# Optimization experiments

Measured on AMD Instinct MI355X. Metric: run time of the kernel, lower is better.

Reference implementation:

```python
import jax, jax.numpy as jnp
import numpy as np

N_EMBD = 1024
BLOCK_SIZE = 2048
ATTN_SPAN = 256
LN_EPS = 1e-5


def _band_mask(T, span, dtype):
    ones = jnp.ones((T, T), dtype=dtype)
    # tril(.,0) * (1 - tril(.,-span)) -> causal band of width `span`
    return jnp.tril(ones, 0) * (1.0 - jnp.tril(ones, -span))


def setup_inputs() -> dict:
    key = jax.random.key(0)
    k_x, k_w, k_b, k_lw = jax.random.split(key, 4)
    B, T, C = 4, BLOCK_SIZE, N_EMBD
    x = jax.random.normal(k_x, (B, T, C), dtype=jnp.float32)
    # qkv_net: Linear(C, 3C) with bias (torch default)
    lim = 1.0 / np.sqrt(C)
    W_qkv = jax.random.uniform(k_w, (C, 3 * C), minval=-lim, maxval=lim, dtype=jnp.float32)
    b_qkv = jax.random.uniform(k_b, (3 * C,), minval=-lim, maxval=lim, dtype=jnp.float32)
    ln_w = jnp.ones((C,), dtype=jnp.float32)
    ln_b = jnp.zeros((C,), dtype=jnp.float32)
    return {"x": x, "W_qkv": W_qkv, "b_qkv": b_qkv, "ln_w": ln_w, "ln_b": ln_b}


def _layer_norm(h, w, b):
    mu = jnp.mean(h, axis=-1, keepdims=True)
    var = jnp.var(h, axis=-1, keepdims=True)
    return (h - mu) * jax.lax.rsqrt(var + LN_EPS) * w + b


def reference(x, W_qkv, b_qkv, ln_w, ln_b):
    B, T, C = x.shape
    qkv = x @ W_qkv + b_qkv  # [B,T,3C]
    q, k, v = jnp.split(qkv, 3, axis=-1)
    scale = np.sqrt(C * ATTN_SPAN).astype(np.float32)
    scores = jnp.einsum('bid,bjd->bij', q, k) / scale  # [B,T,T]
    scores = scores * _band_mask(T, ATTN_SPAN, x.dtype)[None, :, :]
    out = jnp.einsum('bij,bjd->bid', scores, v)  # [B,T,C]
    return _layer_norm(out, ln_w, ln_b)
```

## Files before the change

kernel.cpp:

```cpp
#include <hip/hip_runtime.h>
#include <cstdint>
#include <cstddef>

#define N_EMBD 1024
#define T_SEQ  2048
#define NBATCH 4
#define SPAN   256
#define C3     3072

typedef float  floatx4 __attribute__((ext_vector_type(4)));
typedef __bf16 bf16x8  __attribute__((ext_vector_type(8)));

__device__ inline unsigned short f2bf(float f) {
    union { float f; unsigned u; } x; x.f = f;
    unsigned u = x.u;
    unsigned r = (u + 0x7fffu + ((u >> 16) & 1u)) >> 16;
    return (unsigned short)r;
}

typedef __attribute__((address_space(1))) const void GVOID;
typedef __attribute__((address_space(3))) void LVOID;
__device__ inline void gl2lds16(const void* g, void* l) {
    __builtin_amdgcn_global_load_lds((GVOID*)g, (LVOID*)l, 16, 0, 0);
}

__device__ inline void stage128x32(const unsigned short* g, size_t stride,
                                   unsigned short* lds, int lane, int wave) {
    const int r     = wave * 16 + (lane >> 2);
    const int chunk = (lane & 3) ^ ((r >> 1) & 3);
    const unsigned short* src = g + (size_t)r * stride + chunk * 8;
    gl2lds16(src,               &lds[(wave * 16) * 32]);
    gl2lds16(src + 64 * stride, &lds[(64 + wave * 16) * 32]);
}

__device__ inline void stage64x64(const unsigned short* g, size_t stride,
                                  unsigned short* lds, int lane, int wave) {
#pragma unroll
    for (int rnd = 0; rnd < 2; rnd++) {
        const int r = rnd * 32 + wave * 8 + (lane >> 3);
        const int chunk = (lane & 7) ^ (r & 7);
        gl2lds16(g + (size_t)r * stride + chunk * 8, &lds[(rnd * 32 + wave * 8) * 64]);
    }
}

__device__ inline void stage128x64(const unsigned short* g, size_t stride,
                                   unsigned short* lds, int lane, int wave) {
#pragma unroll
    for (int rnd = 0; rnd < 4; rnd++) {
        const int r = rnd * 32 + wave * 8 + (lane >> 3);
        const int chunk = (lane & 7) ^ (r & 7);
        gl2lds16(g + (size_t)r * stride + chunk * 8, &lds[(rnd * 32 + wave * 8) * 64]);
    }
}

__global__ __launch_bounds__(256) void k_prep(const float* __restrict__ x,
                                              unsigned short* __restrict__ Xb,
                                              const float* __restrict__ W,
                                              unsigned short* __restrict__ WbT) {
    __shared__ unsigned short t[32][33];
    if (blockIdx.x < 8192) {
        int i = (blockIdx.x * 256 + threadIdx.x) * 4;
        float4 v = *(const float4*)(x + i);
        ushort4 o;
        o.x = f2bf(v.x); o.y = f2bf(v.y); o.z = f2bf(v.z); o.w = f2bf(v.w);
        *(ushort4*)(Xb + i) = o;
    } else {
        int bid = blockIdx.x - 8192;
        int k0 = (bid & 31) * 32, n0 = (bid >> 5) * 32;
        int tx = threadIdx.x & 31, ty = threadIdx.x >> 5;
#pragma unroll
        for (int i = 0; i < 4; i++) {
            int k = k0 + ty + i * 8;
            t[ty + i * 8][tx] = f2bf(W[(size_t)k * C3 + n0 + tx]);
        }
        __syncthreads();
#pragma unroll
        for (int i = 0; i < 4; i++) {
            int n = n0 + ty + i * 8;
            WbT[(size_t)n * N_EMBD + k0 + tx] = t[tx][ty + i * 8];
        }
    }
}

__global__ __launch_bounds__(256) void k_gemm(const unsigned short* __restrict__ Xb,
                                              const unsigned short* __restrict__ WbT,
                                              const float* __restrict__ bqkv,
                                              unsigned short* __restrict__ QK,
                                              unsigned short* __restrict__ Vt) {
    __shared__ unsigned short As[4096];
    __shared__ unsigned short Bs[4096];
    const int tid = threadIdx.x, lane = tid & 63, wave = tid >> 6;
    const int bx = blockIdx.x, m0 = blockIdx.y * 128;
    const bool isV = (bx >= 16);
    const int n0 = isV ? (2048 + (bx - 16) * 128) : (bx * 128);
    const int wr = wave >> 1, wc = wave & 1;

    floatx4 acc[4][4] = {};

    const unsigned short* gA = (isV ? WbT + (size_t)n0 * N_EMBD : Xb  + (size_t)m0 * N_EMBD);
    const unsigned short* gB = (isV ? Xb  + (size_t)m0 * N_EMBD : WbT + (size_t)n0 * N_EMBD);
    const int qk = ((lane >> 4) ^ ((lane >> 1) & 3)) * 8;
    const int ra = wr * 64 + (lane & 15);
    const int rb = wc * 64 + (lane & 15);

    for (int k0 = 0; k0 < N_EMBD; k0 += 32) {
        stage128x32(gA + k0, N_EMBD, As, lane, wave);
        stage128x32(gB + k0, N_EMBD, Bs, lane, wave);
        __syncthreads();
        bf16x8 a[4], b[4];
#pragma unroll
        for (int mi = 0; mi < 4; mi++) a[mi] = *(const bf16x8*)&As[(ra + mi * 16) * 32 + qk];
#pragma unroll
        for (int ni = 0; ni < 4; ni++) b[ni] = *(const bf16x8*)&Bs[(rb + ni * 16) * 32 + qk];
#pragma unroll
        for (int mi = 0; mi < 4; mi++)
#pragma unroll
            for (int ni = 0; ni < 4; ni++)
                acc[mi][ni] = __builtin_amdgcn_mfma_f32_16x16x32_bf16(a[mi], b[ni], acc[mi][ni], 0, 0, 0);
        __syncthreads();
    }

    const int cn = lane & 15, q = lane >> 4;
    unsigned short* base = isV ? Vt : QK;
    const int rowbase = isV ? (((m0 >> 11) << 10) + (n0 - 2048)) : m0;
    const int colbase = isV ? (m0 & 2047) : n0;
#pragma unroll
    for (int mi = 0; mi < 4; mi++) {
#pragma unroll
        for (int r = 0; r < 4; r++) {
            const int arow = wr * 64 + mi * 16 + q * 4 + r;
            unsigned short* dst = base + (size_t)(rowbase + arow) * 2048 + colbase;
#pragma unroll
            for (int ni = 0; ni < 4; ni++) {
                const int acol = wc * 64 + ni * 16 + cn;
                const float bias = bqkv[n0 + (isV ? arow : acol)];
                dst[acol] = f2bf(acc[mi][ni][r] + bias);
            }
        }
    }
}

__global__ __launch_bounds__(256) void k_scores(const unsigned short* __restrict__ QK,
                                                unsigned short* __restrict__ S) {
    const int jj = blockIdx.x, qb = blockIdx.y, b = blockIdx.z;
    const int jb = qb - 4 + jj;
    if (jb < 0) return;

    __shared__ unsigned short Qs[4096];
    __shared__ unsigned short Ks[4096];
    const int tid = threadIdx.x, lane = tid & 63, wave = tid >> 6;
    const int wr = wave >> 1, wc = wave & 1;
    const int n15 = lane & 15, q = lane >> 4;

    floatx4 acc[2][2] = {};

    const unsigned short* gQ = QK + ((size_t)(b * T_SEQ + qb * 64)) * 2048;
    const unsigned short* gK = QK + ((size_t)(b * T_SEQ + jb * 64)) * 2048 + 1024;

    for (int k0 = 0; k0 < N_EMBD; k0 += 64) {
        stage64x64(gQ + k0, 2048, Qs, lane, wave);
        stage64x64(gK + k0, 2048, Ks, lane, wave);
        __syncthreads();
#pragma unroll
        for (int s = 0; s < 2; s++) {
            bf16x8 a[2], bbf[2];
#pragma unroll
            for (int mi = 0; mi < 2; mi++) {
                const int row = wr * 32 + mi * 16 + n15;
                a[mi] = *(const bf16x8*)&Qs[row * 64 + (((s * 4 + q) ^ (row & 7)) * 8)];
            }
#pragma unroll
            for (int ni = 0; ni < 2; ni++) {
                const int row = wc * 32 + ni * 16 + n15;
                bbf[ni] = *(const bf16x8*)&Ks[row * 64 + (((s * 4 + q) ^ (row & 7)) * 8)];
            }
#pragma unroll
            for (int mi = 0; mi < 2; mi++)
#pragma unroll
                for (int ni = 0; ni < 2; ni++)
                    acc[mi][ni] = __builtin_amdgcn_mfma_f32_16x16x32_bf16(a[mi], bbf[ni], acc[mi][ni], 0, 0, 0);
        }
        __syncthreads();
    }

    unsigned short* Sb = S + (((size_t)(b * 32 + qb) * 5 + jj) << 12);
#pragma unroll
    for (int mi = 0; mi < 2; mi++)
#pragma unroll
        for (int ni = 0; ni < 2; ni++)
#pragma unroll
            for (int r = 0; r < 4; r++) {
                const int il = wr * 32 + mi * 16 + q * 4 + r;
                const int jl = wc * 32 + ni * 16 + n15;
                const int gi = qb * 64 + il, gj = jb * 64 + jl;
                const float v = ((gj <= gi) && (gj > gi - SPAN)) ? acc[mi][ni][r] * (1.0f / 512.0f) : 0.0f;
                Sb[il * 64 + jl] = f2bf(v);
            }
}

__global__ __launch_bounds__(256) void k_sv(const unsigned short* __restrict__ S,
                                            const unsigned short* __restrict__ Vt,
                                            float* __restrict__ out) {
    const int cg = blockIdx.x, qb = blockIdx.y, b = blockIdx.z;
    const int c0 = cg * 128;

    __shared__ unsigned short Ss[4096];
    __shared__ unsigned short Vs[8192];
    const int tid = threadIdx.x, lane = tid & 63, wave = tid >> 6;
    const int wr = wave >> 1, wc = wave & 1;
    const int n15 = lane & 15, q = lane >> 4;

    floatx4 acc[2][4] = {};

    for (int jj = 0; jj < 5; jj++) {
        const int jb = qb - 4 + jj;
        if (jb < 0) continue;
        stage64x64(S + (((size_t)(b * 32 + qb) * 5 + jj) << 12), 64, Ss, lane, wave);
        stage128x64(Vt + ((size_t)(b * 1024 + c0)) * 2048 + jb * 64, 2048, Vs, lane, wave);
        __syncthreads();
#pragma unroll
        for (int s = 0; s < 2; s++) {
            bf16x8 a[2], bbf[4];
#pragma unroll
            for (int mi = 0; mi < 2; mi++) {
                const int row = wr * 32 + mi * 16 + n15;
                a[mi] = *(const bf16x8*)&Ss[row * 64 + (((s * 4 + q) ^ (row & 7)) * 8)];
            }
#pragma unroll
            for (int ni = 0; ni < 4; ni++) {
                const int row = wc * 64 + ni * 16 + n15;
                bbf[ni] = *(const bf16x8*)&Vs[row * 64 + (((s * 4 + q) ^ (row & 7)) * 8)];
            }
#pragma unroll
            for (int mi = 0; mi < 2; mi++)
#pragma unroll
                for (int ni = 0; ni < 4; ni++)
                    acc[mi][ni] = __builtin_amdgcn_mfma_f32_16x16x32_bf16(a[mi], bbf[ni], acc[mi][ni], 0, 0, 0);
        }
        __syncthreads();
    }

#pragma unroll
    for (int mi = 0; mi < 2; mi++)
#pragma unroll
        for (int ni = 0; ni < 4; ni++)
#pragma unroll
            for (int r = 0; r < 4; r++) {
                const int il = wr * 32 + mi * 16 + q * 4 + r;
                const int cl = wc * 64 + ni * 16 + n15;
                out[((size_t)(b * T_SEQ + qb * 64 + il)) * N_EMBD + c0 + cl] = acc[mi][ni][r];
            }
}

__global__ __launch_bounds__(256) void k_ln(float* __restrict__ out,
                                            const float* __restrict__ w,
                                            const float* __restrict__ bias) {
    __shared__ float red[8];
    const int t = threadIdx.x;
    float* p = out + (size_t)blockIdx.x * N_EMBD;
    float4 v = ((const float4*)p)[t];
    float s  = v.x + v.y + v.z + v.w;
    float sq = v.x * v.x + v.y * v.y + v.z * v.z + v.w * v.w;
#pragma unroll
    for (int off = 32; off; off >>= 1) {
        s  += __shfl_down(s, off, 64);
        sq += __shfl_down(sq, off, 64);
    }
    const int wave = t >> 6, lane = t & 63;
    if (lane == 0) { red[wave] = s; red[4 + wave] = sq; }
    __syncthreads();
    const float ts = red[0] + red[1] + red[2] + red[3];
    const float tq = red[4] + red[5] + red[6] + red[7];
    const float mean = ts * (1.0f / N_EMBD);
    const float var  = tq * (1.0f / N_EMBD) - mean * mean;
    const float rs = rsqrtf(var + 1e-5f);
    float4 wv = ((const float4*)w)[t];
    float4 bv = ((const float4*)bias)[t];
    float4 o;
    o.x = (v.x - mean) * rs * wv.x + bv.x;
    o.y = (v.y - mean) * rs * wv.y + bv.y;
    o.z = (v.z - mean) * rs * wv.z + bv.z;
    o.w = (v.w - mean) * rs * wv.w + bv.w;
    ((float4*)p)[t] = o;
}

extern "C" void kernel_launch(void* const* d_in, const int* in_sizes, int n_in,
                              void* d_out, int out_size, void* d_ws, size_t ws_size,
                              hipStream_t stream) {
    const float* x  = (const float*)d_in[0];
    const float* W  = (const float*)d_in[1];
    const float* bq = (const float*)d_in[2];
    const float* lw = (const float*)d_in[3];
    const float* lb = (const float*)d_in[4];
    float* out = (float*)d_out;
    char* ws = (char*)d_ws;

    unsigned short* Xb   = (unsigned short*)(ws + 0);
    unsigned short* Sbuf = (unsigned short*)(ws + 0);
    unsigned short* WbT  = (unsigned short*)(ws + 16777216);
    unsigned short* QK   = (unsigned short*)(ws + 23068672);
    unsigned short* Vt   = (unsigned short*)(ws + 56623104);

    k_prep   <<<11264,           256, 0, stream>>>(x, Xb, W, WbT);
    k_gemm   <<<dim3(24, 64),    256, 0, stream>>>(Xb, WbT, bq, QK, Vt);
    k_scores <<<dim3(5, 32, 4),  256, 0, stream>>>(QK, Sbuf);
    k_sv     <<<dim3(8, 32, 4),  256, 0, stream>>>(Sbuf, Vt, out);
    k_ln     <<<8192,            256, 0, stream>>>(out, lw, lb);
}
```

Measured before the change: 207.5 us.

## Rewrite QKV GEMM with 256x128 tiles, double-buffered LDS and interleaved MFMA

The QKV projection GEMM moves from a single-buffered 128x128 tile with K=32 steps and 256 threads to a 256x128 tile with 512 threads. It uses K=64 steps and double-buffered LDS, issuing async global-to-LDS loads between MFMA groups with setprio and sched barriers. A workgroup index remap spreads tiles across XCDs. The aim is to hide global-load latency behind matrix math and raise arithmetic intensity. In exchange it brings a larger LDS footprint (96KB), more barriers, and hand-tuned vmcnt waits that must be exactly right.

Result: slower. 235.1 us (+13.3%).

```diff
diff --git a/kernel.cpp b/kernel.cpp
--- a/kernel.cpp
+++ b/kernel.cpp
@@ -24,13 +24,22 @@
     __builtin_amdgcn_global_load_lds((GVOID*)g, (LVOID*)l, 16, 0, 0);
 }
 
-__device__ inline void stage128x32(const unsigned short* g, size_t stride,
-                                   unsigned short* lds, int lane, int wave) {
-    const int r     = wave * 16 + (lane >> 2);
-    const int chunk = (lane & 3) ^ ((r >> 1) & 3);
-    const unsigned short* src = g + (size_t)r * stride + chunk * 8;
-    gl2lds16(src,               &lds[(wave * 16) * 32]);
-    gl2lds16(src + 64 * stride, &lds[(64 + wave * 16) * 32]);
+
+__device__ inline void stage_half128(const unsigned short* g, size_t stride,
+                                     unsigned short* lds, int lane, int wave) {
+#pragma unroll
+    for (int rnd = 0; rnd < 2; rnd++) {
+        const int r = rnd * 64 + wave * 8 + (lane >> 3);
+        const int chunk = (lane & 7) ^ (r & 7);
+        gl2lds16(g + (size_t)r * stride + chunk * 8, &lds[(rnd * 64 + wave * 8) * 64]);
+    }
+}
+
+__device__ inline void stage_half64(const unsigned short* g, size_t stride,
+                                    unsigned short* lds, int lane, int wave) {
+    const int r = wave * 8 + (lane >> 3);
+    const int chunk = (lane & 7) ^ (r & 7);
+    gl2lds16(g + (size_t)r * stride + chunk * 8, &lds[(wave * 8) * 64]);
 }
 
 __device__ inline void stage64x64(const unsigned short* g, size_t stride,
@@ -51,6 +60,10 @@
         const int chunk = (lane & 7) ^ (r & 7);
         gl2lds16(g + (size_t)r * stride + chunk * 8, &lds[(rnd * 32 + wave * 8) * 64]);
     }
+}
+
+__device__ inline bf16x8 frag_ld(const unsigned short* buf, int row, int ks, int q) {
+    return *(const bf16x8*)&buf[row * 64 + (((ks * 4 + q) ^ (row & 7)) * 8)];
 }
 
 __global__ __launch_bounds__(256) void k_prep(const float* __restrict__ x,
@@ -82,58 +95,154 @@
     }
 }
 
-__global__ __launch_bounds__(256) void k_gemm(const unsigned short* __restrict__ Xb,
+__global__ __launch_bounds__(512) void k_gemm(const unsigned short* __restrict__ Xb,
                                               const unsigned short* __restrict__ WbT,
                                               const float* __restrict__ bqkv,
                                               unsigned short* __restrict__ QK,
                                               unsigned short* __restrict__ Vt) {
-    __shared__ unsigned short As[4096];
-    __shared__ unsigned short Bs[4096];
+    __shared__ unsigned short As[2][256 * 64];
+    __shared__ unsigned short Bs[2][128 * 64];
     const int tid = threadIdx.x, lane = tid & 63, wave = tid >> 6;
-    const int bx = blockIdx.x, m0 = blockIdx.y * 128;
-    const bool isV = (bx >= 16);
-    const int n0 = isV ? (2048 + (bx - 16) * 128) : (bx * 128);
-    const int wr = wave >> 1, wc = wave & 1;
-
-    floatx4 acc[4][4] = {};
-
-    const unsigned short* gA = (isV ? WbT + (size_t)n0 * N_EMBD : Xb  + (size_t)m0 * N_EMBD);
-    const unsigned short* gB = (isV ? Xb  + (size_t)m0 * N_EMBD : WbT + (size_t)n0 * N_EMBD);
-    const int qk = ((lane >> 4) ^ ((lane >> 1) & 3)) * 8;
-    const int ra = wr * 64 + (lane & 15);
-    const int rb = wc * 64 + (lane & 15);
-
-    for (int k0 = 0; k0 < N_EMBD; k0 += 32) {
-        stage128x32(gA + k0, N_EMBD, As, lane, wave);
-        stage128x32(gB + k0, N_EMBD, Bs, lane, wave);
-        __syncthreads();
-        bf16x8 a[4], b[4];
-#pragma unroll
-        for (int mi = 0; mi < 4; mi++) a[mi] = *(const bf16x8*)&As[(ra + mi * 16) * 32 + qk];
-#pragma unroll
-        for (int ni = 0; ni < 4; ni++) b[ni] = *(const bf16x8*)&Bs[(rb + ni * 16) * 32 + qk];
-#pragma unroll
-        for (int mi = 0; mi < 4; mi++)
-#pragma unroll
-            for (int ni = 0; ni < 4; ni++)
-                acc[mi][ni] = __builtin_amdgcn_mfma_f32_16x16x32_bf16(a[mi], b[ni], acc[mi][ni], 0, 0, 0);
-        __syncthreads();
-    }
-
-    const int cn = lane & 15, q = lane >> 4;
+    const int wm = wave >> 2, wn = wave & 3;
+    const int n15 = lane & 15, q = lane >> 4;
+
+    const int wg = (blockIdx.x & 7) * 96 + (blockIdx.x >> 3);
+    const bool isV = (wg >= 512);
+
+    const unsigned short* gA;
+    const unsigned short* gB;
+    int rowbase, colbase, nb;
+    if (!isV) {
+        const int mt = wg >> 4, nt = wg & 15;
+        gA = Xb + (size_t)(mt * 256) * N_EMBD;
+        gB = WbT + (size_t)(nt * 128) * N_EMBD;
+        rowbase = mt * 256; colbase = nt * 128; nb = nt * 128;
+    } else {
+        const int v = wg - 512;
+        const int ct = v >> 6, tv = v & 63;
+        const int t0 = tv * 128;
+        gA = WbT + (size_t)(2048 + ct * 256) * N_EMBD;
+        gB = Xb + (size_t)t0 * N_EMBD;
+        rowbase = (t0 >> 11) * 1024 + ct * 256;
+        colbase = t0 & 2047;
+        nb = 2048 + ct * 256;
+    }
+
+    floatx4 acc[8][2] = {};
+
+#define BAR __builtin_amdgcn_s_barrier()
+#define MFMA8(MIBASE, NI)                                                          \
+    __builtin_amdgcn_sched_barrier(0);                                             \
+    __builtin_amdgcn_s_setprio(1);                                                 \
+    _Pragma("unroll")                                                              \
+    for (int ks = 0; ks < 2; ++ks)                                                 \
+        _Pragma("unroll")                                                          \
+        for (int mi = 0; mi < 4; ++mi)                                             \
+            acc[(MIBASE) + mi][NI] = __builtin_amdgcn_mfma_f32_16x16x32_bf16(      \
+                a[mi][ks], b[NI][ks], acc[(MIBASE) + mi][NI], 0, 0, 0);            \
+    __builtin_amdgcn_s_setprio(0);                                                 \
+    __builtin_amdgcn_sched_barrier(0);
+
+    stage_half128(gA,                    N_EMBD, As[0],            lane, wave);
+    stage_half128(gA + 128 * N_EMBD,     N_EMBD, As[0] + 128 * 64, lane, wave);
+    stage_half64 (gB,                    N_EMBD, Bs[0],            lane, wave);
+    stage_half64 (gB + 64 * N_EMBD,      N_EMBD, Bs[0] + 64 * 64,  lane, wave);
+    stage_half64 (gB + 64,               N_EMBD, Bs[1],            lane, wave);
+    stage_half64 (gB + 64 + 64 * N_EMBD, N_EMBD, Bs[1] + 64 * 64,  lane, wave);
+    asm volatile("s_waitcnt vmcnt(2)" ::: "memory");
+    BAR;
+
+#pragma unroll 1
+    for (int it = 0; it < 8; ++it) {
+        const int t0k = it * 128;
+        const int t1k = t0k + 64;
+        const bool last = (it == 7);
+        bf16x8 a[4][2], b[2][2];
+
+#pragma unroll
+        for (int mi = 0; mi < 4; ++mi)
+#pragma unroll
+            for (int ks = 0; ks < 2; ++ks)
+                a[mi][ks] = frag_ld(As[0], wm * 128 + mi * 16 + n15, ks, q);
+#pragma unroll
+        for (int ks = 0; ks < 2; ++ks)
+            b[0][ks] = frag_ld(Bs[0], wn * 32 + n15, ks, q);
+        stage_half128(gA + t1k, N_EMBD, As[1], lane, wave);
+        BAR;
+        MFMA8(0, 0)
+        BAR;
+#pragma unroll
+        for (int ks = 0; ks < 2; ++ks)
+            b[1][ks] = frag_ld(Bs[0], wn * 32 + 16 + n15, ks, q);
+        stage_half128(gA + t1k + 128 * N_EMBD, N_EMBD, As[1] + 128 * 64, lane, wave);
+        BAR;
+        MFMA8(0, 1)
+        BAR;
+#pragma unroll
+        for (int mi = 0; mi < 4; ++mi)
+#pragma unroll
+            for (int ks = 0; ks < 2; ++ks)
+                a[mi][ks] = frag_ld(As[0], wm * 128 + (mi + 4) * 16 + n15, ks, q);
+        if (!last) stage_half64(gB + t0k + 128, N_EMBD, Bs[0], lane, wave);
+        BAR;
+        MFMA8(4, 1)
+        BAR;
+        if (!last) stage_half64(gB + t0k + 128 + 64 * N_EMBD, N_EMBD, Bs[0] + 64 * 64, lane, wave);
+        BAR;
+        MFMA8(4, 0)
+        if (last) { asm volatile("s_waitcnt vmcnt(0)" ::: "memory"); }
+        else      { asm volatile("s_waitcnt vmcnt(2)" ::: "memory"); }
+        BAR;
+
+#pragma unroll
+        for (int mi = 0; mi < 4; ++mi)
+#pragma unroll
+            for (int ks = 0; ks < 2; ++ks)
+                a[mi][ks] = frag_ld(As[1], wm * 128 + mi * 16 + n15, ks, q);
+#pragma unroll
+        for (int ks = 0; ks < 2; ++ks)
+            b[0][ks] = frag_ld(Bs[1], wn * 32 + n15, ks, q);
+        if (!last) stage_half128(gA + t0k + 128, N_EMBD, As[0], lane, wave);
+        BAR;
+        MFMA8(0, 0)
+        BAR;
+#pragma unroll
+        for (int ks = 0; ks < 2; ++ks)
+            b[1][ks] = frag_ld(Bs[1], wn * 32 + 16 + n15, ks, q);
+        if (!last) stage_half128(gA + t0k + 128 + 128 * N_EMBD, N_EMBD, As[0] + 128 * 64, lane, wave);
+        BAR;
+        MFMA8(0, 1)
+        BAR;
+#pragma unroll
+        for (int mi = 0; mi < 4; ++mi)
+#pragma unroll
+            for (int ks = 0; ks < 2; ++ks)
+                a[mi][ks] = frag_ld(As[1], wm * 128 + (mi + 4) * 16 + n15, ks, q);
+        if (!last) stage_half64(gB + t1k + 128, N_EMBD, Bs[1], lane, wave);
+        BAR;
+        MFMA8(4, 1)
+        BAR;
+        if (!last) stage_half64(gB + t1k + 128 + 64 * N_EMBD, N_EMBD, Bs[1] + 64 * 64, lane, wave);
+        BAR;
+        MFMA8(4, 0)
+        if (!last) { asm volatile("s_waitcnt vmcnt(2)" ::: "memory"); }
+        BAR;
+    }
+#undef MFMA8
+#undef BAR
+
     unsigned short* base = isV ? Vt : QK;
-    const int rowbase = isV ? (((m0 >> 11) << 10) + (n0 - 2048)) : m0;
-    const int colbase = isV ? (m0 & 2047) : n0;
-#pragma unroll
-    for (int mi = 0; mi < 4; mi++) {
-#pragma unroll
-        for (int r = 0; r < 4; r++) {
-            const int arow = wr * 64 + mi * 16 + q * 4 + r;
+#pragma unroll
+    for (int mi = 0; mi < 8; ++mi) {
+#pragma unroll
+        for (int r = 0; r < 4; ++r) {
+            const int arow = wm * 128 + mi * 16 + q * 4 + r;
             unsigned short* dst = base + (size_t)(rowbase + arow) * 2048 + colbase;
-#pragma unroll
-            for (int ni = 0; ni < 4; ni++) {
-                const int acol = wc * 64 + ni * 16 + cn;
-                const float bias = bqkv[n0 + (isV ? arow : acol)];
+            const float rbias = bqkv[nb + arow];
+#pragma unroll
+            for (int ni = 0; ni < 2; ++ni) {
+                const int acol = wn * 32 + ni * 16 + n15;
+                const float bias = isV ? rbias : bqkv[nb + acol];
                 dst[acol] = f2bf(acc[mi][ni][r] + bias);
             }
         }
@@ -302,7 +411,7 @@
     unsigned short* Vt   = (unsigned short*)(ws + 56623104);
 
     k_prep   <<<11264,           256, 0, stream>>>(x, Xb, W, WbT);
-    k_gemm   <<<dim3(24, 64),    256, 0, stream>>>(Xb, WbT, bq, QK, Vt);
+    k_gemm   <<<768,             512, 0, stream>>>(Xb, WbT, bq, QK, Vt);
     k_scores <<<dim3(5, 32, 4),  256, 0, stream>>>(QK, Sbuf);
     k_sv     <<<dim3(8, 32, 4),  256, 0, stream>>>(Sbuf, Vt, out);
     k_ln     <<<8192,            256, 0, stream>>>(out, lw, lb);
```

## Double K-step per barrier and remap block IDs for XCD locality in attention kernels

Applied to the files above, without the earlier changes.

The scores and SV kernels now stage two 64-wide K chunks (or two key blocks) per synchronization, halving barrier count and doubling LDS use. Both grids are flattened to 1D with a swizzle that groups consecutive logical blocks onto the same XCD (blockIdx & 7), aiming to improve L2 reuse of shared Q/K/V tiles. The larger LDS footprint may reduce occupancy.

New measurement: 195.8 us. 5.6% less time.

```diff
diff --git a/kernel.cpp b/kernel.cpp
--- a/kernel.cpp
+++ b/kernel.cpp
@@ -142,12 +142,15 @@
 
 __global__ __launch_bounds__(256) void k_scores(const unsigned short* __restrict__ QK,
                                                 unsigned short* __restrict__ S) {
-    const int jj = blockIdx.x, qb = blockIdx.y, b = blockIdx.z;
+    const int logical = (blockIdx.x & 7) * 80 + (blockIdx.x >> 3);
+    const int jj = logical % 5;
+    const int qb = (logical / 5) & 31;
+    const int b  = logical / 160;
     const int jb = qb - 4 + jj;
     if (jb < 0) return;
 
-    __shared__ unsigned short Qs[4096];
-    __shared__ unsigned short Ks[4096];
+    __shared__ unsigned short Qs[2][4096];
+    __shared__ unsigned short Ks[2][4096];
     const int tid = threadIdx.x, lane = tid & 63, wave = tid >> 6;
     const int wr = wave >> 1, wc = wave & 1;
     const int n15 = lane & 15, q = lane >> 4;
@@ -157,28 +160,33 @@
     const unsigned short* gQ = QK + ((size_t)(b * T_SEQ + qb * 64)) * 2048;
     const unsigned short* gK = QK + ((size_t)(b * T_SEQ + jb * 64)) * 2048 + 1024;
 
-    for (int k0 = 0; k0 < N_EMBD; k0 += 64) {
-        stage64x64(gQ + k0, 2048, Qs, lane, wave);
-        stage64x64(gK + k0, 2048, Ks, lane, wave);
-        __syncthreads();
-#pragma unroll
-        for (int s = 0; s < 2; s++) {
-            bf16x8 a[2], bbf[2];
-#pragma unroll
-            for (int mi = 0; mi < 2; mi++) {
-                const int row = wr * 32 + mi * 16 + n15;
-                a[mi] = *(const bf16x8*)&Qs[row * 64 + (((s * 4 + q) ^ (row & 7)) * 8)];
-            }
-#pragma unroll
-            for (int ni = 0; ni < 2; ni++) {
-                const int row = wc * 32 + ni * 16 + n15;
-                bbf[ni] = *(const bf16x8*)&Ks[row * 64 + (((s * 4 + q) ^ (row & 7)) * 8)];
-            }
-#pragma unroll
-            for (int mi = 0; mi < 2; mi++)
-#pragma unroll
-                for (int ni = 0; ni < 2; ni++)
-                    acc[mi][ni] = __builtin_amdgcn_mfma_f32_16x16x32_bf16(a[mi], bbf[ni], acc[mi][ni], 0, 0, 0);
+    for (int k0 = 0; k0 < N_EMBD; k0 += 128) {
+        stage64x64(gQ + k0,      2048, Qs[0], lane, wave);
+        stage64x64(gQ + k0 + 64, 2048, Qs[1], lane, wave);
+        stage64x64(gK + k0,      2048, Ks[0], lane, wave);
+        stage64x64(gK + k0 + 64, 2048, Ks[1], lane, wave);
+        __syncthreads();
+#pragma unroll
+        for (int h = 0; h < 2; h++) {
+#pragma unroll
+            for (int s = 0; s < 2; s++) {
+                bf16x8 a[2], bbf[2];
+#pragma unroll
+                for (int mi = 0; mi < 2; mi++) {
+                    const int row = wr * 32 + mi * 16 + n15;
+                    a[mi] = *(const bf16x8*)&Qs[h][row * 64 + (((s * 4 + q) ^ (row & 7)) * 8)];
+                }
+#pragma unroll
+                for (int ni = 0; ni < 2; ni++) {
+                    const int row = wc * 32 + ni * 16 + n15;
+                    bbf[ni] = *(const bf16x8*)&Ks[h][row * 64 + (((s * 4 + q) ^ (row & 7)) * 8)];
+                }
+#pragma unroll
+                for (int mi = 0; mi < 2; mi++)
+#pragma unroll
+                    for (int ni = 0; ni < 2; ni++)
+                        acc[mi][ni] = __builtin_amdgcn_mfma_f32_16x16x32_bf16(a[mi], bbf[ni], acc[mi][ni], 0, 0, 0);
+            }
         }
         __syncthreads();
     }
@@ -201,41 +209,57 @@
 __global__ __launch_bounds__(256) void k_sv(const unsigned short* __restrict__ S,
                                             const unsigned short* __restrict__ Vt,
                                             float* __restrict__ out) {
-    const int cg = blockIdx.x, qb = blockIdx.y, b = blockIdx.z;
+    const int logical = (blockIdx.x & 7) * 128 + (blockIdx.x >> 3);
+    const int cg = logical & 7;
+    const int qb = (logical >> 3) & 31;
+    const int b  = logical >> 8;
     const int c0 = cg * 128;
 
-    __shared__ unsigned short Ss[4096];
-    __shared__ unsigned short Vs[8192];
+    __shared__ unsigned short Ss[2][4096];
+    __shared__ unsigned short Vs[2][8192];
     const int tid = threadIdx.x, lane = tid & 63, wave = tid >> 6;
     const int wr = wave >> 1, wc = wave & 1;
     const int n15 = lane & 15, q = lane >> 4;
 
     floatx4 acc[2][4] = {};
 
-    for (int jj = 0; jj < 5; jj++) {
-        const int jb = qb - 4 + jj;
-        if (jb < 0) continue;
-        stage64x64(S + (((size_t)(b * 32 + qb) * 5 + jj) << 12), 64, Ss, lane, wave);
-        stage128x64(Vt + ((size_t)(b * 1024 + c0)) * 2048 + jb * 64, 2048, Vs, lane, wave);
-        __syncthreads();
-#pragma unroll
-        for (int s = 0; s < 2; s++) {
-            bf16x8 a[2], bbf[4];
-#pragma unroll
-            for (int mi = 0; mi < 2; mi++) {
-                const int row = wr * 32 + mi * 16 + n15;
-                a[mi] = *(const bf16x8*)&Ss[row * 64 + (((s * 4 + q) ^ (row & 7)) * 8)];
-            }
-#pragma unroll
-            for (int ni = 0; ni < 4; ni++) {
-                const int row = wc * 64 + ni * 16 + n15;
-                bbf[ni] = *(const bf16x8*)&Vs[row * 64 + (((s * 4 + q) ^ (row & 7)) * 8)];
-            }
-#pragma unroll
-            for (int mi = 0; mi < 2; mi++)
-#pragma unroll
-                for (int ni = 0; ni < 4; ni++)
-                    acc[mi][ni] = __builtin_amdgcn_mfma_f32_16x16x32_bf16(a[mi], bbf[ni], acc[mi][ni], 0, 0, 0);
+    const size_t vbase = ((size_t)(b * 1024 + c0)) * 2048;
+    const size_t sbase = ((size_t)(b * 32 + qb) * 5) << 12;
+
+    for (int j0 = 0; j0 < 5; j0 += 2) {
+        const int nv = (j0 < 4) ? 2 : 1;
+        bool val[2] = {false, false};
+#pragma unroll
+        for (int t = 0; t < 2; t++) {
+            if (t < nv && (qb - 4 + j0 + t) >= 0) {
+                val[t] = true;
+                stage64x64 (S + sbase + ((size_t)(j0 + t) << 12), 64, Ss[t], lane, wave);
+                stage128x64(Vt + vbase + (size_t)(qb - 4 + j0 + t) * 64, 2048, Vs[t], lane, wave);
+            }
+        }
+        __syncthreads();
+#pragma unroll
+        for (int t = 0; t < 2; t++) {
+            if (!val[t]) continue;
+#pragma unroll
+            for (int s = 0; s < 2; s++) {
+                bf16x8 a[2], bbf[4];
+#pragma unroll
+                for (int mi = 0; mi < 2; mi++) {
+                    const int row = wr * 32 + mi * 16 + n15;
+                    a[mi] = *(const bf16x8*)&Ss[t][row * 64 + (((s * 4 + q) ^ (row & 7)) * 8)];
+                }
+#pragma unroll
+                for (int ni = 0; ni < 4; ni++) {
+                    const int row = wc * 64 + ni * 16 + n15;
+                    bbf[ni] = *(const bf16x8*)&Vs[t][row * 64 + (((s * 4 + q) ^ (row & 7)) * 8)];
+                }
+#pragma unroll
+                for (int mi = 0; mi < 2; mi++)
+#pragma unroll
+                    for (int ni = 0; ni < 4; ni++)
+                        acc[mi][ni] = __builtin_amdgcn_mfma_f32_16x16x32_bf16(a[mi], bbf[ni], acc[mi][ni], 0, 0, 0);
+            }
         }
         __syncthreads();
     }
@@ -303,7 +327,7 @@
 
     k_prep   <<<11264,           256, 0, stream>>>(x, Xb, W, WbT);
     k_gemm   <<<dim3(24, 64),    256, 0, stream>>>(Xb, WbT, bq, QK, Vt);
-    k_scores <<<dim3(5, 32, 4),  256, 0, stream>>>(QK, Sbuf);
-    k_sv     <<<dim3(8, 32, 4),  256, 0, stream>>>(Sbuf, Vt, out);
+    k_scores <<<640,             256, 0, stream>>>(QK, Sbuf);
+    k_sv     <<<1024,            256, 0, stream>>>(Sbuf, Vt, out);
     k_ln     <<<8192,            256, 0, stream>>>(out, lw, lb);
 }
```

## Fuse scores, score-times-V and layernorm into one attention kernel

Applied to the files above, without the earlier changes.

Replaces the separate scores, S·V and layernorm kernels with a single k_attn kernel. Each block owns 32 query rows, computes the banded scores against five K tiles with double-buffered LDS staging, keeps the masked scores in LDS, then multiplies by V straight from global memory and applies layernorm in registers. This removes the S round trip through global memory, the fp32 output reread for layernorm, and two launches. In exchange the grid drops to 256 blocks, each holding a large accumulator (acc_o 2x16 floatx4) and using about 80KB of LDS, so occupancy is low and V loads are uncached global reads.

Result: slower. 225.1 us (+8.5%).

```diff
diff --git a/kernel.cpp b/kernel.cpp
--- a/kernel.cpp
+++ b/kernel.cpp
@@ -43,14 +43,15 @@
     }
 }
 
-__device__ inline void stage128x64(const unsigned short* g, size_t stride,
-                                   unsigned short* lds, int lane, int wave) {
-#pragma unroll
-    for (int rnd = 0; rnd < 4; rnd++) {
-        const int r = rnd * 32 + wave * 8 + (lane >> 3);
-        const int chunk = (lane & 7) ^ (r & 7);
-        gl2lds16(g + (size_t)r * stride + chunk * 8, &lds[(rnd * 32 + wave * 8) * 64]);
-    }
+__device__ inline void stage32x64(const unsigned short* g, size_t stride,
+                                  unsigned short* lds, int lane, int wave) {
+    const int r = wave * 8 + (lane >> 3);
+    const int chunk = (lane & 7) ^ (r & 7);
+    gl2lds16(g + (size_t)r * stride + chunk * 8, &lds[(wave * 8) * 64]);
+}
+
+__device__ inline bf16x8 frag_ld(const unsigned short* buf, int row, int ks, int q) {
+    return *(const bf16x8*)&buf[row * 64 + (((ks * 4 + q) ^ (row & 7)) * 8)];
 }
 
 __global__ __launch_bounds__(256) void k_prep(const float* __restrict__ x,
@@ -140,148 +141,146 @@
     }
 }
 
-__global__ __launch_bounds__(256) void k_scores(const unsigned short* __restrict__ QK,
-                                                unsigned short* __restrict__ S) {
-    const int jj = blockIdx.x, qb = blockIdx.y, b = blockIdx.z;
-    const int jb = qb - 4 + jj;
-    if (jb < 0) return;
-
-    __shared__ unsigned short Qs[4096];
-    __shared__ unsigned short Ks[4096];
+__global__ __launch_bounds__(256) void k_attn(const unsigned short* __restrict__ QK,
+                                              const unsigned short* __restrict__ Vt,
+                                              const float* __restrict__ lw,
+                                              const float* __restrict__ lb,
+                                              float* __restrict__ out) {
+    const int qh = blockIdx.x, b = blockIdx.y;
+    const int r0 = qh * 32;
+    const int jt0 = (qh >> 1) - 4;
+
+    __shared__ unsigned short Qd[2][32 * 64];
+    __shared__ unsigned short Kd[2][5 * 64 * 64];
+    __shared__ unsigned short Ss[5][32 * 64];
+    __shared__ float red[2][32][4];
+
     const int tid = threadIdx.x, lane = tid & 63, wave = tid >> 6;
-    const int wr = wave >> 1, wc = wave & 1;
     const int n15 = lane & 15, q = lane >> 4;
 
-    floatx4 acc[2][2] = {};
-
-    const unsigned short* gQ = QK + ((size_t)(b * T_SEQ + qb * 64)) * 2048;
-    const unsigned short* gK = QK + ((size_t)(b * T_SEQ + jb * 64)) * 2048 + 1024;
-
-    for (int k0 = 0; k0 < N_EMBD; k0 += 64) {
-        stage64x64(gQ + k0, 2048, Qs, lane, wave);
-        stage64x64(gK + k0, 2048, Ks, lane, wave);
+    const unsigned short* gQ = QK + (size_t)(b * T_SEQ + r0) * 2048;
+
+    floatx4 acc_s[2][5] = {};
+
+    stage32x64(gQ, 2048, Qd[0], lane, wave);
+#pragma unroll
+    for (int jtl = 0; jtl < 5; ++jtl) {
+        const int jt = jt0 + jtl;
+        if (jt >= 0)
+            stage64x64(QK + (size_t)(b * T_SEQ + jt * 64) * 2048 + 1024,
+                       2048, Kd[0] + jtl * 4096, lane, wave);
+    }
+    __syncthreads();
+
+#pragma unroll 1
+    for (int kst = 0; kst < 16; ++kst) {
+        const int cur = kst & 1;
+        if (kst < 15) {
+            const int kc = (kst + 1) * 64;
+            stage32x64(gQ + kc, 2048, Qd[cur ^ 1], lane, wave);
+#pragma unroll
+            for (int jtl = 0; jtl < 5; ++jtl) {
+                const int jt = jt0 + jtl;
+                if (jt >= 0)
+                    stage64x64(QK + (size_t)(b * T_SEQ + jt * 64) * 2048 + 1024 + kc,
+                               2048, Kd[cur ^ 1] + jtl * 4096, lane, wave);
+            }
+        }
+#pragma unroll
+        for (int ks = 0; ks < 2; ++ks) {
+            bf16x8 a0 = frag_ld(Qd[cur], n15, ks, q);
+            bf16x8 a1 = frag_ld(Qd[cur], 16 + n15, ks, q);
+#pragma unroll
+            for (int jtl = 0; jtl < 5; ++jtl) {
+                if (jt0 + jtl < 0) continue;
+                bf16x8 bk = frag_ld(Kd[cur] + jtl * 4096, wave * 16 + n15, ks, q);
+                acc_s[0][jtl] = __builtin_amdgcn_mfma_f32_16x16x32_bf16(a0, bk, acc_s[0][jtl], 0, 0, 0);
+                acc_s[1][jtl] = __builtin_amdgcn_mfma_f32_16x16x32_bf16(a1, bk, acc_s[1][jtl], 0, 0, 0);
+            }
+        }
         __syncthreads();
-#pragma unroll
-        for (int s = 0; s < 2; s++) {
-            bf16x8 a[2], bbf[2];
-#pragma unroll
-            for (int mi = 0; mi < 2; mi++) {
-                const int row = wr * 32 + mi * 16 + n15;
-                a[mi] = *(const bf16x8*)&Qs[row * 64 + (((s * 4 + q) ^ (row & 7)) * 8)];
-            }
-#pragma unroll
-            for (int ni = 0; ni < 2; ni++) {
-                const int row = wc * 32 + ni * 16 + n15;
-                bbf[ni] = *(const bf16x8*)&Ks[row * 64 + (((s * 4 + q) ^ (row & 7)) * 8)];
-            }
-#pragma unroll
-            for (int mi = 0; mi < 2; mi++)
-#pragma unroll
-                for (int ni = 0; ni < 2; ni++)
-                    acc[mi][ni] = __builtin_amdgcn_mfma_f32_16x16x32_bf16(a[mi], bbf[ni], acc[mi][ni], 0, 0, 0);
-        }
-        __syncthreads();
-    }
-
-    unsigned short* Sb = S + (((size_t)(b * 32 + qb) * 5 + jj) << 12);
-#pragma unroll
-    for (int mi = 0; mi < 2; mi++)
-#pragma unroll
-        for (int ni = 0; ni < 2; ni++)
-#pragma unroll
-            for (int r = 0; r < 4; r++) {
-                const int il = wr * 32 + mi * 16 + q * 4 + r;
-                const int jl = wc * 32 + ni * 16 + n15;
-                const int gi = qb * 64 + il, gj = jb * 64 + jl;
-                const float v = ((gj <= gi) && (gj > gi - SPAN)) ? acc[mi][ni][r] * (1.0f / 512.0f) : 0.0f;
-                Sb[il * 64 + jl] = f2bf(v);
-            }
-}
-
-__global__ __launch_bounds__(256) void k_sv(const unsigned short* __restrict__ S,
-                                            const unsigned short* __restrict__ Vt,
-                                            float* __restrict__ out) {
-    const int cg = blockIdx.x, qb = blockIdx.y, b = blockIdx.z;
-    const int c0 = cg * 128;
-
-    __shared__ unsigned short Ss[4096];
-    __shared__ unsigned short Vs[8192];
-    const int tid = threadIdx.x, lane = tid & 63, wave = tid >> 6;
-    const int wr = wave >> 1, wc = wave & 1;
-    const int n15 = lane & 15, q = lane >> 4;
-
-    floatx4 acc[2][4] = {};
-
-    for (int jj = 0; jj < 5; jj++) {
-        const int jb = qb - 4 + jj;
-        if (jb < 0) continue;
-        stage64x64(S + (((size_t)(b * 32 + qb) * 5 + jj) << 12), 64, Ss, lane, wave);
-        stage128x64(Vt + ((size_t)(b * 1024 + c0)) * 2048 + jb * 64, 2048, Vs, lane, wave);
-        __syncthreads();
-#pragma unroll
-        for (int s = 0; s < 2; s++) {
-            bf16x8 a[2], bbf[4];
-#pragma unroll
-            for (int mi = 0; mi < 2; mi++) {
-                const int row = wr * 32 + mi * 16 + n15;
-                a[mi] = *(const bf16x8*)&Ss[row * 64 + (((s * 4 + q) ^ (row & 7)) * 8)];
-            }
-#pragma unroll
-            for (int ni = 0; ni < 4; ni++) {
-                const int row = wc * 64 + ni * 16 + n15;
-                bbf[ni] = *(const bf16x8*)&Vs[row * 64 + (((s * 4 + q) ^ (row & 7)) * 8)];
-            }
-#pragma unroll
-            for (int mi = 0; mi < 2; mi++)
-#pragma unroll
-                for (int ni = 0; ni < 4; ni++)
-                    acc[mi][ni] = __builtin_amdgcn_mfma_f32_16x16x32_bf16(a[mi], bbf[ni], acc[mi][ni], 0, 0, 0);
-        }
-        __syncthreads();
-    }
-
-#pragma unroll
-    for (int mi = 0; mi < 2; mi++)
-#pragma unroll
-        for (int ni = 0; ni < 4; ni++)
-#pragma unroll
-            for (int r = 0; r < 4; r++) {
-                const int il = wr * 32 + mi * 16 + q * 4 + r;
-                const int cl = wc * 64 + ni * 16 + n15;
-                out[((size_t)(b * T_SEQ + qb * 64 + il)) * N_EMBD + c0 + cl] = acc[mi][ni][r];
-            }
-}
-
-__global__ __launch_bounds__(256) void k_ln(float* __restrict__ out,
-                                            const float* __restrict__ w,
-                                            const float* __restrict__ bias) {
-    __shared__ float red[8];
-    const int t = threadIdx.x;
-    float* p = out + (size_t)blockIdx.x * N_EMBD;
-    float4 v = ((const float4*)p)[t];
-    float s  = v.x + v.y + v.z + v.w;
-    float sq = v.x * v.x + v.y * v.y + v.z * v.z + v.w * v.w;
-#pragma unroll
-    for (int off = 32; off; off >>= 1) {
-        s  += __shfl_down(s, off, 64);
-        sq += __shfl_down(sq, off, 64);
-    }
-    const int wave = t >> 6, lane = t & 63;
-    if (lane == 0) { red[wave] = s; red[4 + wave] = sq; }
+    }
+
+    {
+        const int jl = wave * 16 + n15;
+#pragma unroll
+        for (int jtl = 0; jtl < 5; ++jtl) {
+            const int jt = jt0 + jtl;
+            if (jt < 0) continue;
+            const int gj = jt * 64 + jl;
+#pragma unroll
+            for (int mi = 0; mi < 2; ++mi)
+#pragma unroll
+                for (int r = 0; r < 4; ++r) {
+                    const int il = mi * 16 + q * 4 + r;
+                    const int gi = r0 + il;
+                    const float v = ((gj <= gi) && (gj > gi - SPAN))
+                                        ? acc_s[mi][jtl][r] * (1.0f / 512.0f) : 0.0f;
+                    Ss[jtl][il * 64 + (((jl >> 3) ^ (il & 7)) * 8) + (jl & 7)] = f2bf(v);
+                }
+        }
+    }
     __syncthreads();
-    const float ts = red[0] + red[1] + red[2] + red[3];
-    const float tq = red[4] + red[5] + red[6] + red[7];
-    const float mean = ts * (1.0f / N_EMBD);
-    const float var  = tq * (1.0f / N_EMBD) - mean * mean;
-    const float rs = rsqrtf(var + 1e-5f);
-    float4 wv = ((const float4*)w)[t];
-    float4 bv = ((const float4*)bias)[t];
-    float4 o;
-    o.x = (v.x - mean) * rs * wv.x + bv.x;
-    o.y = (v.y - mean) * rs * wv.y + bv.y;
-    o.z = (v.z - mean) * rs * wv.z + bv.z;
-    o.w = (v.w - mean) * rs * wv.w + bv.w;
-    ((float4*)p)[t] = o;
+
+    floatx4 acc_o[2][16] = {};
+    const unsigned short* gV = Vt + (size_t)(b * 1024 + wave * 256) * 2048;
+#pragma unroll
+    for (int jtl = 0; jtl < 5; ++jtl) {
+        const int jt = jt0 + jtl;
+        if (jt < 0) continue;
+#pragma unroll
+        for (int ks = 0; ks < 2; ++ks) {
+            bf16x8 a0 = frag_ld(Ss[jtl], n15, ks, q);
+            bf16x8 a1 = frag_ld(Ss[jtl], 16 + n15, ks, q);
+            const size_t tb = (size_t)jt * 64 + ks * 32 + q * 8;
+#pragma unroll
+            for (int nt = 0; nt < 16; ++nt) {
+                const bf16x8 bv = *(const bf16x8*)(gV + (size_t)(nt * 16 + n15) * 2048 + tb);
+                acc_o[0][nt] = __builtin_amdgcn_mfma_f32_16x16x32_bf16(a0, bv, acc_o[0][nt], 0, 0, 0);
+                acc_o[1][nt] = __builtin_amdgcn_mfma_f32_16x16x32_bf16(a1, bv, acc_o[1][nt], 0, 0, 0);
+            }
+        }
+    }
+
+#pragma unroll
+    for (int mi = 0; mi < 2; ++mi)
+#pragma unroll
+        for (int r = 0; r < 4; ++r) {
+            float s = 0.0f, sq = 0.0f;
+#pragma unroll
+            for (int nt = 0; nt < 16; ++nt) {
+                const float v = acc_o[mi][nt][r];
+                s += v; sq += v * v;
+            }
+#pragma unroll
+            for (int off = 1; off < 16; off <<= 1) {
+                s  += __shfl_xor(s, off, 64);
+                sq += __shfl_xor(sq, off, 64);
+            }
+            if (n15 == 0) {
+                red[0][mi * 16 + q * 4 + r][wave] = s;
+                red[1][mi * 16 + q * 4 + r][wave] = sq;
+            }
+        }
+    __syncthreads();
+
+    float* po = out + (size_t)(b * T_SEQ + r0) * N_EMBD;
+#pragma unroll
+    for (int mi = 0; mi < 2; ++mi)
+#pragma unroll
+        for (int r = 0; r < 4; ++r) {
+            const int row = mi * 16 + q * 4 + r;
+            const float ts = red[0][row][0] + red[0][row][1] + red[0][row][2] + red[0][row][3];
+            const float tq = red[1][row][0] + red[1][row][1] + red[1][row][2] + red[1][row][3];
+            const float mean = ts * (1.0f / N_EMBD);
+            const float var  = tq * (1.0f / N_EMBD) - mean * mean;
+            const float rs = rsqrtf(var + 1e-5f);
+#pragma unroll
+            for (int nt = 0; nt < 16; ++nt) {
+                const int c = wave * 256 + nt * 16 + n15;
+                po[(size_t)row * N_EMBD + c] = (acc_o[mi][nt][r] - mean) * rs * lw[c] + lb[c];
+            }
+        }
 }
 
 extern "C" void kernel_launch(void* const* d_in, const int* in_sizes, int n_in,
@@ -296,14 +295,11 @@
     char* ws = (char*)d_ws;
 
     unsigned short* Xb   = (unsigned short*)(ws + 0);
-    unsigned short* Sbuf = (unsigned short*)(ws + 0);
     unsigned short* WbT  = (unsigned short*)(ws + 16777216);
     unsigned short* QK   = (unsigned short*)(ws + 23068672);
     unsigned short* Vt   = (unsigned short*)(ws + 56623104);
 
-    k_prep   <<<11264,           256, 0, stream>>>(x, Xb, W, WbT);
-    k_gemm   <<<dim3(24, 64),    256, 0, stream>>>(Xb, WbT, bq, QK, Vt);
-    k_scores <<<dim3(5, 32, 4),  256, 0, stream>>>(QK, Sbuf);
-    k_sv     <<<dim3(8, 32, 4),  256, 0, stream>>>(Sbuf, Vt, out);
-    k_ln     <<<8192,            256, 0, stream>>>(out, lw, lb);
-}
+    k_prep <<<11264,        256, 0, stream>>>(x, Xb, W, WbT);
+    k_gemm <<<dim3(24, 64), 256, 0, stream>>>(Xb, WbT, bq, QK, Vt);
+    k_attn <<<dim3(64, 4),  256, 0, stream>>>(QK, Vt, lw, lb, out);
+}
```
